# Performance work log

Hardware: AMD Instinct MI355X
Metric: run time of the kernel (lower is better)

## Reference

```python
import jax, jax.numpy as jnp
import numpy as np

DIM = 16        # lagrangian.dim -> y has 2*DIM phase-space coords
HID = 128       # hidden width of the parametric Lagrangian
BATCH = 32768


def setup_inputs() -> dict:
    key = jax.random.key(0)
    k1, k2, k3, k4 = jax.random.split(key, 4)
    y = jax.random.normal(k1, (BATCH, 2 * DIM), dtype=jnp.float32)
    # small-scale init keeps J_{qdot,qdot} = I + (MLP Hessian block) well conditioned
    W1 = jax.random.normal(k2, (HID, 2 * DIM), dtype=jnp.float32) * (1.0 / np.sqrt(2 * DIM))
    b1 = jax.random.normal(k3, (HID,), dtype=jnp.float32) * 0.1
    w2 = jax.random.normal(k4, (HID,), dtype=jnp.float32) * 0.1
    return {"y": y, "W1": W1, "b1": b1, "w2": w2}


def _lagrangian(y_vec, W1, b1, w2):
    """Scalar Lagrangian L(q, qdot) for a single phase-space vector y_vec [2*DIM]."""
    qdot = y_vec[DIM:]
    kinetic = 0.5 * jnp.dot(qdot, qdot)
    return kinetic + jnp.dot(w2, jnp.tanh(W1 @ y_vec + b1))


def reference(y, W1, b1, w2):
    """Acceleration qdotdot = (dL/dq - qdot . J_{q,qdot}) . J_{qdot,qdot}^{-1}.

    Instead of the original O(dim^2) repeated tf.gradients calls, compute the
    full gradient and Hessian once per sample via fused forward-over-reverse
    autodiff, vmapped over the batch.
    """
    d = DIM
    L = lambda yv: _lagrangian(yv, W1, b1, w2)
    grad_fn = jax.grad(L)
    hess_fn = jax.jacfwd(grad_fn)  # forward-over-reverse Hessian, one sweep

    g = jax.vmap(grad_fn)(y)   # [B, 2d]   full dL/dy
    H = jax.vmap(hess_fn)(y)   # [B, 2d, 2d]  full Hessian d2L/(dy dy)

    qdot = y[:, d:]            # [B, d]
    dLdq = g[:, :d]            # [B, d]
    J_qqdot = H[:, :d, d:]     # [B, d, d]  d2L/(dq_i dqdot_j)
    J_qdqd_inv = jnp.linalg.inv(H[:, d:, d:])  # [B, d, d]

    rhs = dLdq - jnp.einsum('bi,bij->bj', qdot, J_qqdot)
    qdotdot = jnp.einsum('bi,bij->bj', rhs, J_qdqd_inv)
    return qdotdot
```

## Files before the change

### kernel.cpp

```cpp
#include <hip/hip_runtime.h>
#include <math.h>

#define DIMQ 16
#define HID  128
#define SPB  16
#define NTHREADS 256

typedef __attribute__((ext_vector_type(8))) _Float16 f16x8;
typedef __attribute__((ext_vector_type(4))) _Float16 f16x4;
typedef __attribute__((ext_vector_type(4))) float f32x4;
typedef __attribute__((ext_vector_type(2))) float v2f;

#define ASTR 280
#define USTR 280
#define SSTR 136

#define OFF_WFF  0
#define OFF_YFF  8192
#define OFF_ABT  9216
#define OFF_USP  18176
#define OFF_SST  27136
#define OFF_MSCR 0
#define LDS_BYTES 31488

__device__ __forceinline__ int mswz(int s, int off) {
    return s * 320 + (off ^ ((s & 7) << 2));
}
__device__ __forceinline__ f16x8 pack8(float4 a, float4 b) {
    f16x8 r;
    r[0]=(_Float16)a.x; r[1]=(_Float16)a.y; r[2]=(_Float16)a.z; r[3]=(_Float16)a.w;
    r[4]=(_Float16)b.x; r[5]=(_Float16)b.y; r[6]=(_Float16)b.z; r[7]=(_Float16)b.w;
    return r;
}

__global__ __launch_bounds__(NTHREADS, 4)
void lag_accel_kernel(const float* __restrict__ y,
                      const float* __restrict__ W1,
                      const float* __restrict__ b1,
                      const float* __restrict__ w2,
                      float* __restrict__ out)
{
    __shared__ __align__(16) char smem[LDS_BYTES];
    _Float16* Wff = (_Float16*)(smem + OFF_WFF);
    _Float16* Yff = (_Float16*)(smem + OFF_YFF);
    _Float16* ABT = (_Float16*)(smem + OFF_ABT);
    _Float16* usp = (_Float16*)(smem + OFF_USP);
    _Float16* sst = (_Float16*)(smem + OFF_SST);

    const int tid = threadIdx.x;
    const long long s0 = (long long)blockIdx.x * SPB;

#pragma unroll
    for (int it = 0; it < 2; ++it) {
        const int slot = tid + it * 256;
        const int ht_ = slot >> 6, grp_ = (slot >> 4) & 3, j_ = slot & 15;
        const float4* src = (const float4*)(W1 + (ht_ * 16 + j_) * 32 + (grp_ << 3));
        *(f16x8*)&Wff[slot * 8] = pack8(src[0], src[1]);
    }
    if (tid < 128) {
        const int grp_ = (tid >> 5) & 3, j_ = (tid >> 1) & 15, hf = tid & 1;
        float4 v = *(const float4*)(y + (s0 + j_) * 32 + (grp_ << 3) + (hf << 2));
        f16x4 p; p[0]=(_Float16)v.x; p[1]=(_Float16)v.y; p[2]=(_Float16)v.z; p[3]=(_Float16)v.w;
        *(f16x4*)&Yff[((grp_ * 16 + j_) << 3) + (hf << 2)] = p;
    }
#pragma unroll
    for (int it = 0; it < 2; ++it) {
        const int idx = tid + it * 256;
        const int k = idx & 31, h0 = (idx >> 5) << 3;
        float v[8];
#pragma unroll
        for (int i = 0; i < 8; ++i) v[i] = W1[(h0 + i) * 32 + k];
        f16x8 p;
#pragma unroll
        for (int i = 0; i < 8; ++i) p[i] = (_Float16)v[i];
        const int j_ = (k < 16) ? k : (k - 16);
        const int off = (k < 16) ? h0 : (128 + h0);
        *(f16x8*)&ABT[j_ * ASTR + off] = p;
    }

    const int wave = tid >> 6;
    const int lane = tid & 63;
    const int grp  = lane >> 4;
    const int j    = lane & 15;

    __syncthreads();

    f16x8 yf = *(const f16x8*)&Yff[((grp * 16 + j) << 3)];

    f32x4 zacc[2], aacc[2];
    float4 w2v[2];
#pragma unroll
    for (int t = 0; t < 2; ++t) {
        const int ht = wave * 2 + t;
        f16x8 aW  = *(const f16x8*)&Wff[((ht * 4 + grp) * 16 + j) * 8];
        f16x8 aAl = *(const f16x8*)&Wff[((ht * 4 + (grp & 1)) * 16 + j) * 8];
        f16x8 aA;
#pragma unroll
        for (int e = 0; e < 8; ++e) aA[e] = (grp >= 2) ? aAl[e] : (_Float16)0.0f;
        float4 b1v = *(const float4*)&b1[ht * 16 + (grp << 2)];
        w2v[t] = *(const float4*)&w2[ht * 16 + (grp << 2)];
        f32x4 ci; ci[0] = b1v.x; ci[1] = b1v.y; ci[2] = b1v.z; ci[3] = b1v.w;
        f32x4 zf = {0.0f, 0.0f, 0.0f, 0.0f};
        zacc[t] = __builtin_amdgcn_mfma_f32_16x16x32_f16(aW, yf, ci, 0, 0, 0);
        aacc[t] = __builtin_amdgcn_mfma_f32_16x16x32_f16(aA, yf, zf, 0, 0, 0);
    }

#define EWST(t)                                                          \
    {                                                                    \
        const int h4 = (wave * 2 + (t)) * 16 + (grp << 2);               \
        _Float16 su[4], sn[4], sv[4];                                    \
        _Pragma("unroll")                                                \
        for (int r = 0; r < 4; ++r) {                                    \
            float z  = zacc[t][r], aq = aacc[t][r];                      \
            float w2c = (r == 0) ? w2v[t].x : (r == 1) ? w2v[t].y         \
                       : (r == 2) ? w2v[t].z : w2v[t].w;                 \
            float e  = __expf(2.0f * z);                                 \
            float rr = 2.0f * __builtin_amdgcn_rcpf(e + 1.0f);           \
            float t_ = 1.0f - rr;                                        \
            float u  = w2c * (rr * (2.0f - rr));                         \
            float s  = -2.0f * t_ * u;                                   \
            float sp = s * aq;                                           \
            su[r] = (_Float16)u; sn[r] = (_Float16)(-sp);                \
            sv[r] = (_Float16)s;                                         \
        }                                                                \
        f16x4 pa = {su[0], su[1], su[2], su[3]};                         \
        f16x4 pb = {sn[0], sn[1], sn[2], sn[3]};                         \
        f16x4 pc = {sv[0], sv[1], sv[2], sv[3]};                         \
        *(f16x4*)&usp[j * USTR + h4]       = pa;                         \
        *(f16x4*)&usp[j * USTR + 128 + h4] = pb;                         \
        *(f16x4*)&sst[j * SSTR + h4]       = pc;                         \
    }
    EWST(0)
    EWST(1)
#undef EWST

    __syncthreads();

    f32x4 racc = {0.0f, 0.0f, 0.0f, 0.0f};
    if (wave == 0) {
#pragma unroll
        for (int kc = 0; kc < 8; ++kc) {
            f16x8 af = *(const f16x8*)&ABT[j * ASTR + (kc << 5) + (grp << 3)];
            f16x8 bf = *(const f16x8*)&usp[j * USTR + (kc << 5) + (grp << 3)];
            racc = __builtin_amdgcn_mfma_f32_16x16x32_f16(af, bf, racc, 0, 0, 0);
        }
    }

    f32x4 acc[4];
    {
        f32x4 ident;
#pragma unroll
        for (int r = 0; r < 4; ++r) ident[r] = ((grp << 2) + r == j) ? 1.0f : 0.0f;
#pragma unroll
        for (int gs = 0; gs < 4; ++gs) acc[gs] = ident;
    }
#pragma unroll
    for (int kc = 0; kc < 4; ++kc) {
        f16x8 bfrag = *(const f16x8*)&ABT[j * ASTR + 128 + (kc << 5) + (grp << 3)];
#pragma unroll
        for (int gs = 0; gs < 4; ++gs) {
            f16x8 sfrag = *(const f16x8*)&sst[(wave * 4 + gs) * SSTR + (kc << 5) + (grp << 3)];
            f16x8 afrag = sfrag * bfrag;
            acc[gs] = __builtin_amdgcn_mfma_f32_16x16x32_f16(afrag, bfrag, acc[gs], 0, 0, 0);
        }
    }

    __syncthreads();

    float* Mscr = (float*)(smem + OFF_MSCR);
#pragma unroll
    for (int gs = 0; gs < 4; ++gs) {
        float4 v;
        v.x = acc[gs][0]; v.y = acc[gs][1]; v.z = acc[gs][2]; v.w = acc[gs][3];
        *(float4*)&Mscr[mswz(wave * 4 + gs, j * 20 + (grp << 2))] = v;
    }

    __syncthreads();

    if (wave != 0) return;
    const int sl = lane & 15;
    const int rb = lane >> 4;

    v2f M2[4][8];
    float r4[4], d4[4];
#pragma unroll
    for (int r = 0; r < 4; ++r) {
        const int ro = (4 * rb + r) * 20;
        float4 v0 = *(const float4*)&Mscr[mswz(sl, ro + 0)];
        float4 v1 = *(const float4*)&Mscr[mswz(sl, ro + 4)];
        float4 v2 = *(const float4*)&Mscr[mswz(sl, ro + 8)];
        float4 v3 = *(const float4*)&Mscr[mswz(sl, ro + 12)];
        M2[r][0] = (v2f){v0.x, v0.y}; M2[r][1] = (v2f){v0.z, v0.w};
        M2[r][2] = (v2f){v1.x, v1.y}; M2[r][3] = (v2f){v1.z, v1.w};
        M2[r][4] = (v2f){v2.x, v2.y}; M2[r][5] = (v2f){v2.z, v2.w};
        M2[r][6] = (v2f){v3.x, v3.y}; M2[r][7] = (v2f){v3.z, v3.w};
        r4[r] = racc[r];
        d4[r] = 1.0f;
    }

#pragma unroll
    for (int k = 0; k < 16; ++k) {
        const int src = sl + ((k >> 2) << 4);
        float piv = __shfl(M2[k & 3][k >> 1][k & 1], src, 64);
        float rk  = __shfl(r4[k & 3], src, 64);
        float invp = __builtin_amdgcn_rcpf(piv);
        invp = invp * (2.0f - piv * invp);
        float f[4];
#pragma unroll
        for (int r = 0; r < 4; ++r) {
            float fr = M2[r][k >> 1][k & 1] * invp;
            const bool isk = ((rb << 2) + r) == k;
            f[r]  = isk ? 0.0f : fr;
            d4[r] = isk ? piv : d4[r];
            r4[r] = fmaf(-f[r], rk, r4[r]);
        }
        const int i2s = (k >> 1) + (k & 1);
#pragma unroll
        for (int i2 = i2s; i2 < 8; ++i2) {
            float p0 = (2 * i2 == k) ? piv : __shfl(M2[k & 3][i2][0], src, 64);
            float p1 = __shfl(M2[k & 3][i2][1], src, 64);
            v2f pv = {p0, p1};
#pragma unroll
            for (int r = 0; r < 4; ++r) {
                v2f fv = {-f[r], -f[r]};
                M2[r][i2] = __builtin_elementwise_fma(fv, pv, M2[r][i2]);
            }
        }
    }

    float4 xo;
    {
        float i0 = __builtin_amdgcn_rcpf(d4[0]); i0 = i0 * (2.0f - d4[0] * i0);
        float i1 = __builtin_amdgcn_rcpf(d4[1]); i1 = i1 * (2.0f - d4[1] * i1);
        float i2 = __builtin_amdgcn_rcpf(d4[2]); i2 = i2 * (2.0f - d4[2] * i2);
        float i3 = __builtin_amdgcn_rcpf(d4[3]); i3 = i3 * (2.0f - d4[3] * i3);
        xo.x = r4[0] * i0; xo.y = r4[1] * i1; xo.z = r4[2] * i2; xo.w = r4[3] * i3;
    }
    *(float4*)&out[(s0 + sl) * DIMQ + (rb << 2)] = xo;
}

extern "C" void kernel_launch(void* const* d_in, const int* in_sizes, int n_in,
                              void* d_out, int out_size, void* d_ws, size_t ws_size,
                              hipStream_t stream) {
    const float* y  = (const float*)d_in[0];
    const float* W1 = (const float*)d_in[1];
    const float* b1 = (const float*)d_in[2];
    const float* w2 = (const float*)d_in[3];
    float* out = (float*)d_out;
    const int batch = in_sizes[0] / 32;
    const int blocks = (batch + SPB - 1) / SPB;
    lag_accel_kernel<<<blocks, NTHREADS, 0, stream>>>(y, W1, b1, w2, out);
}
```

Baseline: 20.78 us.

## Process 32 samples per block, load y directly into registers, XOR-swizzle LDS

```diff
diff --git a/kernel.cpp b/kernel.cpp
--- a/kernel.cpp
+++ b/kernel.cpp
@@ -3,7 +3,7 @@
 
 #define DIMQ 16
 #define HID  128
-#define SPB  16
+#define SPB  32
 #define NTHREADS 256
 
 typedef __attribute__((ext_vector_type(8))) _Float16 f16x8;
@@ -11,18 +11,14 @@
 typedef __attribute__((ext_vector_type(4))) float f32x4;
 typedef __attribute__((ext_vector_type(2))) float v2f;
 
-#define ASTR 280
-#define USTR 280
-#define SSTR 136
-
 #define OFF_WFF  0
-#define OFF_YFF  8192
-#define OFF_ABT  9216
-#define OFF_USP  18176
-#define OFF_SST  27136
+#define OFF_ABT  8192
+#define OFF_USP  16384
+#define OFF_SST  32768
 #define OFF_MSCR 0
-#define LDS_BYTES 31488
-
+#define LDS_BYTES 40960
+
+__device__ __forceinline__ int axor(int row, int off) { return off ^ ((row & 7) << 3); }
 __device__ __forceinline__ int mswz(int s, int off) {
     return s * 320 + (off ^ ((s & 7) << 2));
 }
@@ -42,13 +38,24 @@
 {
     __shared__ __align__(16) char smem[LDS_BYTES];
     _Float16* Wff = (_Float16*)(smem + OFF_WFF);
-    _Float16* Yff = (_Float16*)(smem + OFF_YFF);
     _Float16* ABT = (_Float16*)(smem + OFF_ABT);
     _Float16* usp = (_Float16*)(smem + OFF_USP);
     _Float16* sst = (_Float16*)(smem + OFF_SST);
 
     const int tid = threadIdx.x;
     const long long s0 = (long long)blockIdx.x * SPB;
+
+    const int wave = tid >> 6;
+    const int lane = tid & 63;
+    const int grp  = lane >> 4;
+    const int j    = lane & 15;
+
+    f16x8 yf[2];
+#pragma unroll
+    for (int st = 0; st < 2; ++st) {
+        const float4* yg = (const float4*)(y + (s0 + st * 16 + j) * 32 + (grp << 3));
+        yf[st] = pack8(yg[0], yg[1]);
+    }
 
 #pragma unroll
     for (int it = 0; it < 2; ++it) {
@@ -57,12 +64,6 @@
         const float4* src = (const float4*)(W1 + (ht_ * 16 + j_) * 32 + (grp_ << 3));
         *(f16x8*)&Wff[slot * 8] = pack8(src[0], src[1]);
     }
-    if (tid < 128) {
-        const int grp_ = (tid >> 5) & 3, j_ = (tid >> 1) & 15, hf = tid & 1;
-        float4 v = *(const float4*)(y + (s0 + j_) * 32 + (grp_ << 3) + (hf << 2));
-        f16x4 p; p[0]=(_Float16)v.x; p[1]=(_Float16)v.y; p[2]=(_Float16)v.z; p[3]=(_Float16)v.w;
-        *(f16x4*)&Yff[((grp_ * 16 + j_) << 3) + (hf << 2)] = p;
-    }
 #pragma unroll
     for (int it = 0; it < 2; ++it) {
         const int idx = tid + it * 256;
@@ -75,19 +76,12 @@
         for (int i = 0; i < 8; ++i) p[i] = (_Float16)v[i];
         const int j_ = (k < 16) ? k : (k - 16);
         const int off = (k < 16) ? h0 : (128 + h0);
-        *(f16x8*)&ABT[j_ * ASTR + off] = p;
-    }
-
-    const int wave = tid >> 6;
-    const int lane = tid & 63;
-    const int grp  = lane >> 4;
-    const int j    = lane & 15;
-
-    __syncthreads();
-
-    f16x8 yf = *(const f16x8*)&Yff[((grp * 16 + j) << 3)];
-
-    f32x4 zacc[2], aacc[2];
+        *(f16x8*)&ABT[(j_ << 8) + axor(j_, off)] = p;
+    }
+
+    __syncthreads();
+
+    f32x4 zacc[2][2], aacc[2][2];
     float4 w2v[2];
 #pragma unroll
     for (int t = 0; t < 2; ++t) {
@@ -101,17 +95,21 @@
         w2v[t] = *(const float4*)&w2[ht * 16 + (grp << 2)];
         f32x4 ci; ci[0] = b1v.x; ci[1] = b1v.y; ci[2] = b1v.z; ci[3] = b1v.w;
         f32x4 zf = {0.0f, 0.0f, 0.0f, 0.0f};
-        zacc[t] = __builtin_amdgcn_mfma_f32_16x16x32_f16(aW, yf, ci, 0, 0, 0);
-        aacc[t] = __builtin_amdgcn_mfma_f32_16x16x32_f16(aA, yf, zf, 0, 0, 0);
-    }
-
-#define EWST(t)                                                          \
+#pragma unroll
+        for (int st = 0; st < 2; ++st) {
+            zacc[t][st] = __builtin_amdgcn_mfma_f32_16x16x32_f16(aW, yf[st], ci, 0, 0, 0);
+            aacc[t][st] = __builtin_amdgcn_mfma_f32_16x16x32_f16(aA, yf[st], zf, 0, 0, 0);
+        }
+    }
+
+#define EWST(t, st)                                                      \
     {                                                                    \
         const int h4 = (wave * 2 + (t)) * 16 + (grp << 2);               \
+        const int smp2 = (st) * 16 + j;                                  \
         _Float16 su[4], sn[4], sv[4];                                    \
         _Pragma("unroll")                                                \
         for (int r = 0; r < 4; ++r) {                                    \
-            float z  = zacc[t][r], aq = aacc[t][r];                      \
+            float z  = zacc[t][st][r], aq = aacc[t][st][r];              \
             float w2c = (r == 0) ? w2v[t].x : (r == 1) ? w2v[t].y         \
                        : (r == 2) ? w2v[t].z : w2v[t].w;                 \
             float e  = __expf(2.0f * z);                                 \
@@ -126,40 +124,43 @@
         f16x4 pa = {su[0], su[1], su[2], su[3]};                         \
         f16x4 pb = {sn[0], sn[1], sn[2], sn[3]};                         \
         f16x4 pc = {sv[0], sv[1], sv[2], sv[3]};                         \
-        *(f16x4*)&usp[j * USTR + h4]       = pa;                         \
-        *(f16x4*)&usp[j * USTR + 128 + h4] = pb;                         \
-        *(f16x4*)&sst[j * SSTR + h4]       = pc;                         \
-    }
-    EWST(0)
-    EWST(1)
+        *(f16x4*)&usp[(smp2 << 8) + axor(smp2, h4)]       = pa;          \
+        *(f16x4*)&usp[(smp2 << 8) + axor(smp2, 128 + h4)] = pb;          \
+        *(f16x4*)&sst[(smp2 << 7) + axor(smp2, h4)]       = pc;          \
+    }
+    EWST(0, 0) EWST(0, 1) EWST(1, 0) EWST(1, 1)
 #undef EWST
 
     __syncthreads();
 
     f32x4 racc = {0.0f, 0.0f, 0.0f, 0.0f};
-    if (wave == 0) {
+    if (wave < 2) {
 #pragma unroll
         for (int kc = 0; kc < 8; ++kc) {
-            f16x8 af = *(const f16x8*)&ABT[j * ASTR + (kc << 5) + (grp << 3)];
-            f16x8 bf = *(const f16x8*)&usp[j * USTR + (kc << 5) + (grp << 3)];
+            const int o = (kc << 5) + (grp << 3);
+            const int smp = wave * 16 + j;
+            f16x8 af = *(const f16x8*)&ABT[(j << 8) + axor(j, o)];
+            f16x8 bf = *(const f16x8*)&usp[(smp << 8) + axor(smp, o)];
             racc = __builtin_amdgcn_mfma_f32_16x16x32_f16(af, bf, racc, 0, 0, 0);
         }
     }
 
-    f32x4 acc[4];
+    f32x4 acc[8];
     {
         f32x4 ident;
 #pragma unroll
         for (int r = 0; r < 4; ++r) ident[r] = ((grp << 2) + r == j) ? 1.0f : 0.0f;
 #pragma unroll
-        for (int gs = 0; gs < 4; ++gs) acc[gs] = ident;
+        for (int gs = 0; gs < 8; ++gs) acc[gs] = ident;
     }
 #pragma unroll
     for (int kc = 0; kc < 4; ++kc) {
-        f16x8 bfrag = *(const f16x8*)&ABT[j * ASTR + 128 + (kc << 5) + (grp << 3)];
-#pragma unroll
-        for (int gs = 0; gs < 4; ++gs) {
-            f16x8 sfrag = *(const f16x8*)&sst[(wave * 4 + gs) * SSTR + (kc << 5) + (grp << 3)];
+        const int o = (kc << 5) + (grp << 3);
+        f16x8 bfrag = *(const f16x8*)&ABT[(j << 8) + axor(j, 128 + o)];
+#pragma unroll
+        for (int gs = 0; gs < 8; ++gs) {
+            const int smp = wave * 8 + gs;
+            f16x8 sfrag = *(const f16x8*)&sst[(smp << 7) + axor(smp, o)];
             f16x8 afrag = sfrag * bfrag;
             acc[gs] = __builtin_amdgcn_mfma_f32_16x16x32_f16(afrag, bfrag, acc[gs], 0, 0, 0);
         }
@@ -169,27 +170,28 @@
 
     float* Mscr = (float*)(smem + OFF_MSCR);
 #pragma unroll
-    for (int gs = 0; gs < 4; ++gs) {
+    for (int gs = 0; gs < 8; ++gs) {
         float4 v;
         v.x = acc[gs][0]; v.y = acc[gs][1]; v.z = acc[gs][2]; v.w = acc[gs][3];
-        *(float4*)&Mscr[mswz(wave * 4 + gs, j * 20 + (grp << 2))] = v;
-    }
-
-    __syncthreads();
-
-    if (wave != 0) return;
+        *(float4*)&Mscr[mswz(wave * 8 + gs, j * 20 + (grp << 2))] = v;
+    }
+
+    __syncthreads();
+
+    if (wave >= 2) return;
     const int sl = lane & 15;
     const int rb = lane >> 4;
+    const int s  = wave * 16 + sl;
 
     v2f M2[4][8];
     float r4[4], d4[4];
 #pragma unroll
     for (int r = 0; r < 4; ++r) {
         const int ro = (4 * rb + r) * 20;
-        float4 v0 = *(const float4*)&Mscr[mswz(sl, ro + 0)];
-        float4 v1 = *(const float4*)&Mscr[mswz(sl, ro + 4)];
-        float4 v2 = *(const float4*)&Mscr[mswz(sl, ro + 8)];
-        float4 v3 = *(const float4*)&Mscr[mswz(sl, ro + 12)];
+        float4 v0 = *(const float4*)&Mscr[mswz(s, ro + 0)];
+        float4 v1 = *(const float4*)&Mscr[mswz(s, ro + 4)];
+        float4 v2 = *(const float4*)&Mscr[mswz(s, ro + 8)];
+        float4 v3 = *(const float4*)&Mscr[mswz(s, ro + 12)];
         M2[r][0] = (v2f){v0.x, v0.y}; M2[r][1] = (v2f){v0.z, v0.w};
         M2[r][2] = (v2f){v1.x, v1.y}; M2[r][3] = (v2f){v1.z, v1.w};
         M2[r][4] = (v2f){v2.x, v2.y}; M2[r][5] = (v2f){v2.z, v2.w};
@@ -236,7 +238,7 @@
         float i3 = __builtin_amdgcn_rcpf(d4[3]); i3 = i3 * (2.0f - d4[3] * i3);
         xo.x = r4[0] * i0; xo.y = r4[1] * i1; xo.z = r4[2] * i2; xo.w = r4[3] * i3;
     }
-    *(float4*)&out[(s0 + sl) * DIMQ + (rb << 2)] = xo;
+    *(float4*)&out[(s0 + s) * DIMQ + (rb << 2)] = xo;
 }
 
 extern "C" void kernel_launch(void* const* d_in, const int* in_sizes, int n_in,
```

Result: faster. 19.57 us (-5.8%).
